# Optimization experiments

Measured on AMD Instinct MI355X. Metric: run time of the kernel, lower is better.

## Reference

```python
import jax, jax.numpy as jnp
import numpy as np

SOFTENING = 0.01
SOFTENING_SQ = SOFTENING * SOFTENING


def setup_inputs() -> dict:
    key = jax.random.key(0)
    k1, k2 = jax.random.split(key)
    N = 8192
    positions = jax.random.normal(k1, (N, 3), dtype=jnp.float32)
    masses = jax.random.uniform(k2, (N,), dtype=jnp.float32)
    return {"positions": positions, "masses": masses}


def reference(positions, masses):
    # diff[i, j] = r_j - r_i  -> shape (N, N, 3)
    diff = positions[None, :, :] - positions[:, None, :]
    dist_sq = jnp.sum(diff * diff, axis=2) + SOFTENING_SQ        # (N, N)
    inv_dist_cubed = dist_sq ** (-1.5)                            # (N, N)
    # a_i = sum_j m_j * diff[i, j] * inv_dist_cubed[i, j]
    w = masses[None, :] * inv_dist_cubed                          # (N, N)
    accelerations = jnp.einsum('ij,ijd->id', w, diff)             # (N, 3)
    return accelerations
```

## Files before the change

### kernel.cpp

```cpp
#include <hip/hip_runtime.h>

#define NBODY 8192
#define BLOCK 256
#define IPT 2
#define ITILE (BLOCK * IPT)
#define NITILES (NBODY / ITILE)
#define SLABS 64
#define JCHUNK (NBODY / SLABS)
#define NF (NBODY * 3)
#define SOFT2 1.0e-4f

__global__ __launch_bounds__(BLOCK) void pack_kernel(
    const float* __restrict__ pos, const float* __restrict__ mass,
    float4* __restrict__ pw) {
  const int i = blockIdx.x * BLOCK + threadIdx.x;
  pw[i] = make_float4(pos[i * 3 + 0], pos[i * 3 + 1], pos[i * 3 + 2], mass[i]);
}

__global__ __launch_bounds__(BLOCK) void force_kernel(
    const float4* __restrict__ pw, float* __restrict__ part) {
  const int t = threadIdx.x;
  const int i1 = blockIdx.x * ITILE + t;
  const int i2 = i1 + BLOCK;
  const int jbase = blockIdx.y * JCHUNK;

  const float4 p1 = pw[i1];
  const float4 p2 = pw[i2];
  const float x1 = p1.x, y1 = p1.y, z1 = p1.z;
  const float x2 = p2.x, y2 = p2.y, z2 = p2.z;

  float ax1 = 0.f, ay1 = 0.f, az1 = 0.f;
  float ax2 = 0.f, ay2 = 0.f, az2 = 0.f;

#pragma unroll 8
  for (int k = 0; k < JCHUNK; ++k) {
    const float4 o = pw[jbase + k];

    float dx1 = o.x - x1, dy1 = o.y - y1, dz1 = o.z - z1;
    float dx2 = o.x - x2, dy2 = o.y - y2, dz2 = o.z - z2;
    float r21 = fmaf(dx1, dx1, fmaf(dy1, dy1, fmaf(dz1, dz1, SOFT2)));
    float r22 = fmaf(dx2, dx2, fmaf(dy2, dy2, fmaf(dz2, dz2, SOFT2)));
    float in1 = __builtin_amdgcn_rsqf(r21);
    float in2 = __builtin_amdgcn_rsqf(r22);
    float w1 = o.w * (in1 * in1 * in1);
    float w2 = o.w * (in2 * in2 * in2);
    ax1 = fmaf(w1, dx1, ax1);
    ay1 = fmaf(w1, dy1, ay1);
    az1 = fmaf(w1, dz1, az1);
    ax2 = fmaf(w2, dx2, ax2);
    ay2 = fmaf(w2, dy2, ay2);
    az2 = fmaf(w2, dz2, az2);
  }

  float* __restrict__ dst = part + (size_t)blockIdx.y * NF;
  dst[i1 * 3 + 0] = ax1;
  dst[i1 * 3 + 1] = ay1;
  dst[i1 * 3 + 2] = az1;
  dst[i2 * 3 + 0] = ax2;
  dst[i2 * 3 + 1] = ay2;
  dst[i2 * 3 + 2] = az2;
}

__global__ __launch_bounds__(BLOCK) void reduce_kernel(
    const float* __restrict__ part, float* __restrict__ out) {
  const int idx = blockIdx.x * BLOCK + threadIdx.x;
  float s = 0.f;
#pragma unroll
  for (int sl = 0; sl < SLABS; ++sl) s += part[(size_t)sl * NF + idx];
  out[idx] = s;
}

extern "C" void kernel_launch(void* const* d_in, const int* in_sizes, int n_in,
                              void* d_out, int out_size, void* d_ws,
                              size_t ws_size, hipStream_t stream) {
  const float* pos = (const float*)d_in[0];
  const float* mass = (const float*)d_in[1];
  float* out = (float*)d_out;

  float4* pw = (float4*)d_ws;
  float* part = (float*)d_ws + (size_t)NBODY * 4;

  pack_kernel<<<NBODY / BLOCK, BLOCK, 0, stream>>>(pos, mass, pw);
  force_kernel<<<dim3(NITILES, SLABS), BLOCK, 0, stream>>>(pw, part);
  reduce_kernel<<<NF / BLOCK, BLOCK, 0, stream>>>(part, out);
}
```

Measured before the change: 96.28 us.

## Fuse packing into force kernel via LDS tile, double slabs, atomic split reduction

Removes the separate pack kernel: each force block stages its 64-body j-chunk (position plus mass) into shared memory and reads its own i positions straight from the input. The slab count doubles to 128, giving more blocks and shorter inner loops. Partial accelerations are now stored component-major so the reduce reads coalesced. The reduce is split four ways across slabs and combined with atomicAdd into an output zeroed by a memset. The costs are twice as much partial-buffer traffic, atomics whose summation order is not deterministic, and an extra memset on the stream.

After: 85.99 us. -10.7%, faster.

```diff
diff --git a/kernel.cpp b/kernel.cpp
--- a/kernel.cpp
+++ b/kernel.cpp
@@ -5,37 +5,41 @@
 #define IPT 2
 #define ITILE (BLOCK * IPT)
 #define NITILES (NBODY / ITILE)
-#define SLABS 64
+#define SLABS 128
 #define JCHUNK (NBODY / SLABS)
 #define NF (NBODY * 3)
 #define SOFT2 1.0e-4f
 
-__global__ __launch_bounds__(BLOCK) void pack_kernel(
+__global__ __launch_bounds__(BLOCK, 8) void force_kernel(
     const float* __restrict__ pos, const float* __restrict__ mass,
-    float4* __restrict__ pw) {
-  const int i = blockIdx.x * BLOCK + threadIdx.x;
-  pw[i] = make_float4(pos[i * 3 + 0], pos[i * 3 + 1], pos[i * 3 + 2], mass[i]);
-}
+    float* __restrict__ part) {
+  __shared__ float4 tile[JCHUNK];
 
-__global__ __launch_bounds__(BLOCK) void force_kernel(
-    const float4* __restrict__ pw, float* __restrict__ part) {
   const int t = threadIdx.x;
+  const int j0 = blockIdx.y * JCHUNK;
+  if (t < JCHUNK) {
+    const int j = j0 + t;
+    tile[t] =
+        make_float4(pos[j * 3 + 0], pos[j * 3 + 1], pos[j * 3 + 2], mass[j]);
+  }
+
   const int i1 = blockIdx.x * ITILE + t;
   const int i2 = i1 + BLOCK;
-  const int jbase = blockIdx.y * JCHUNK;
-
-  const float4 p1 = pw[i1];
-  const float4 p2 = pw[i2];
-  const float x1 = p1.x, y1 = p1.y, z1 = p1.z;
-  const float x2 = p2.x, y2 = p2.y, z2 = p2.z;
+  const float x1 = pos[i1 * 3 + 0];
+  const float y1 = pos[i1 * 3 + 1];
+  const float z1 = pos[i1 * 3 + 2];
+  const float x2 = pos[i2 * 3 + 0];
+  const float y2 = pos[i2 * 3 + 1];
+  const float z2 = pos[i2 * 3 + 2];
 
   float ax1 = 0.f, ay1 = 0.f, az1 = 0.f;
   float ax2 = 0.f, ay2 = 0.f, az2 = 0.f;
 
-#pragma unroll 8
+  __syncthreads();
+
+#pragma unroll 4
   for (int k = 0; k < JCHUNK; ++k) {
-    const float4 o = pw[jbase + k];
-
+    const float4 o = tile[k];
     float dx1 = o.x - x1, dy1 = o.y - y1, dz1 = o.z - z1;
     float dx2 = o.x - x2, dy2 = o.y - y2, dz2 = o.z - z2;
     float r21 = fmaf(dx1, dx1, fmaf(dy1, dy1, fmaf(dz1, dz1, SOFT2)));
@@ -53,21 +57,29 @@
   }
 
   float* __restrict__ dst = part + (size_t)blockIdx.y * NF;
-  dst[i1 * 3 + 0] = ax1;
-  dst[i1 * 3 + 1] = ay1;
-  dst[i1 * 3 + 2] = az1;
-  dst[i2 * 3 + 0] = ax2;
-  dst[i2 * 3 + 1] = ay2;
-  dst[i2 * 3 + 2] = az2;
+  dst[0 * NBODY + i1] = ax1;
+  dst[1 * NBODY + i1] = ay1;
+  dst[2 * NBODY + i1] = az1;
+  dst[0 * NBODY + i2] = ax2;
+  dst[1 * NBODY + i2] = ay2;
+  dst[2 * NBODY + i2] = az2;
 }
 
 __global__ __launch_bounds__(BLOCK) void reduce_kernel(
     const float* __restrict__ part, float* __restrict__ out) {
   const int idx = blockIdx.x * BLOCK + threadIdx.x;
-  float s = 0.f;
-#pragma unroll
-  for (int sl = 0; sl < SLABS; ++sl) s += part[(size_t)sl * NF + idx];
-  out[idx] = s;
+  const int c = idx >> 13;
+  const int b = idx & (NBODY - 1);
+  const int sl0 = blockIdx.y * (SLABS / 4);
+  float s0 = 0.f, s1 = 0.f, s2 = 0.f, s3 = 0.f;
+#pragma unroll 8
+  for (int sl = 0; sl < SLABS / 4; sl += 4) {
+    s0 += part[(size_t)(sl0 + sl + 0) * NF + idx];
+    s1 += part[(size_t)(sl0 + sl + 1) * NF + idx];
+    s2 += part[(size_t)(sl0 + sl + 2) * NF + idx];
+    s3 += part[(size_t)(sl0 + sl + 3) * NF + idx];
+  }
+  atomicAdd(&out[b * 3 + c], (s0 + s1) + (s2 + s3));
 }
 
 extern "C" void kernel_launch(void* const* d_in, const int* in_sizes, int n_in,
@@ -76,11 +88,10 @@
   const float* pos = (const float*)d_in[0];
   const float* mass = (const float*)d_in[1];
   float* out = (float*)d_out;
+  float* part = (float*)d_ws;
 
-  float4* pw = (float4*)d_ws;
-  float* part = (float*)d_ws + (size_t)NBODY * 4;
+  hipMemsetAsync(d_out, 0, (size_t)out_size * sizeof(float), stream);
 
-  pack_kernel<<<NBODY / BLOCK, BLOCK, 0, stream>>>(pos, mass, pw);
-  force_kernel<<<dim3(NITILES, SLABS), BLOCK, 0, stream>>>(pw, part);
-  reduce_kernel<<<NF / BLOCK, BLOCK, 0, stream>>>(part, out);
+  force_kernel<<<dim3(NITILES, SLABS), BLOCK, 0, stream>>>(pos, mass, part);
+  reduce_kernel<<<dim3(NF / BLOCK, 4), BLOCK, 0, stream>>>(part, out);
 }
```
